# Kernel tuning notes

Measured on AMD Instinct MI355X. Metric: run time of the kernel, lower is better.

Reference implementation:

```python
import jax, jax.numpy as jnp
import numpy as np

N = 100000   # nodes
E = 1600000  # edges (avg degree 16)
IN, H, OUT, P = 100, 256, 256, 128
EPS = 1e-5


def setup_inputs() -> dict:
    key = jax.random.key(0)
    ks = jax.random.split(key, 12)

    def lin(k, o, i):
        return jax.random.normal(k, (o, i), jnp.float32) / np.float32(np.sqrt(i))

    return {
        "x": jax.random.normal(ks[0], (N, IN), jnp.float32),
        "edge_index": jax.random.randint(ks[1], (2, E), 0, N),
        # SAGEConv l (aggregated-neighbor branch, has bias) and r (root branch, no bias)
        "Wl0": lin(ks[2], H, IN), "bl0": jnp.zeros((H,), jnp.float32), "Wr0": lin(ks[3], H, IN),
        "Wl1": lin(ks[4], H, H),  "bl1": jnp.zeros((H,), jnp.float32), "Wr1": lin(ks[5], H, H),
        "Wl2": lin(ks[6], OUT, H), "bl2": jnp.zeros((OUT,), jnp.float32), "Wr2": lin(ks[7], OUT, H),
        # projection head + BatchNorm1d(128)
        "Wp": lin(ks[8], P, OUT), "bp": jnp.zeros((P,), jnp.float32),
        "gamma": jnp.ones((P,), jnp.float32), "beta": jnp.zeros((P,), jnp.float32),
    }


def _sage_conv(x, src, dst, Wl, bl, Wr):
    # PyG SAGEConv default: mean-aggregate source features into destinations,
    # then lin_l(agg) + lin_r(x).
    agg = jax.ops.segment_sum(x[src], dst, num_segments=N)           # [N, d]
    deg = jax.ops.segment_sum(jnp.ones((src.shape[0],), x.dtype), dst, num_segments=N)
    agg = agg / jnp.maximum(deg, 1.0)[:, None]
    return agg @ Wl.T + bl + x @ Wr.T


def reference(x, edge_index, Wl0, bl0, Wr0, Wl1, bl1, Wr1, Wl2, bl2, Wr2, Wp, bp, gamma, beta):
    src, dst = edge_index[0], edge_index[1]
    x = jax.nn.relu(_sage_conv(x, src, dst, Wl0, bl0, Wr0))  # dropout is identity in eval
    x = jax.nn.relu(_sage_conv(x, src, dst, Wl1, bl1, Wr1))
    x = _sage_conv(x, src, dst, Wl2, bl2, Wr2)               # no relu on last layer
    z = x @ Wp.T + bp                                        # projection head -> [N, 128]
    mu = jnp.mean(z, axis=0)
    var = jnp.var(z, axis=0)                                 # biased, as torch BN uses for normalization
    h = gamma * (z - mu) * jax.lax.rsqrt(var + EPS) + beta
    return (x, h)
```

## Files before the change

kernel.cpp:

```cpp
#include <hip/hip_runtime.h>
#include <hip/hip_bf16.h>

#define EPS_BN 1e-5f

using short8  = __attribute__((ext_vector_type(8))) short;
using ushort8 = __attribute__((ext_vector_type(8))) unsigned short;
using f32x4   = __attribute__((ext_vector_type(4))) float;

typedef const __attribute__((address_space(1))) void* gas_ptr;
typedef __attribute__((address_space(3))) void* las_ptr;

__device__ inline float bf2f(unsigned short u) {
    union { unsigned i; float f; } c; c.i = ((unsigned)u) << 16; return c.f;
}
__device__ inline unsigned short f2bf(float f) {
    unsigned x = __float_as_uint(f);
    unsigned r = (x + 0x7FFF + ((x >> 16) & 1)) >> 16;
    return (unsigned short)r;
}

__global__ void zero_i32(int* __restrict__ p, int n) {
    int i = blockIdx.x * blockDim.x + threadIdx.x;
    if (i < n) p[i] = 0;
}
__global__ void zero_f32(float* __restrict__ p, int n) {
    int i = blockIdx.x * blockDim.x + threadIdx.x;
    if (i < n) p[i] = 0.0f;
}

__global__ void zero_rows(unsigned short* __restrict__ xpad,
                          unsigned short* __restrict__ h1,
                          unsigned short* __restrict__ h2, int n) {
    int t = threadIdx.x;
    if (t < 128) xpad[(size_t)n * 128 + t] = 0;
    h1[(size_t)n * 256 + t] = 0;
    h2[(size_t)n * 256 + t] = 0;
}

__global__ void conv_w(const float* __restrict__ w, unsigned short* __restrict__ o,
                       int R, int C, int CP) {
    int t = blockIdx.x * blockDim.x + threadIdx.x;
    if (t >= R * CP) return;
    int r = t / CP, c = t % CP;
    o[t] = (c < C) ? f2bf(w[(size_t)r * C + c]) : (unsigned short)0;
}

__global__ void conv_x_pad(const float* __restrict__ x, unsigned short* __restrict__ xp, int n) {
    int t = blockIdx.x * blockDim.x + threadIdx.x;
    if (t >= n * 32) return;
    int node = t >> 5, g = t & 31;
    int f0 = g * 4;
    ushort4 o;
    const float* xr = x + (size_t)node * 100;
    o.x = (f0 + 0 < 100) ? f2bf(xr[f0 + 0]) : 0;
    o.y = (f0 + 1 < 100) ? f2bf(xr[f0 + 1]) : 0;
    o.z = (f0 + 2 < 100) ? f2bf(xr[f0 + 2]) : 0;
    o.w = (f0 + 3 < 100) ? f2bf(xr[f0 + 3]) : 0;
    *(ushort4*)(xp + (size_t)node * 128 + f0) = o;
}

__global__ void count_k(const int* __restrict__ dst, int* __restrict__ counts, int E) {
    int i = blockIdx.x * blockDim.x + threadIdx.x;
    if (i < E) atomicAdd(&counts[dst[i]], 1);
}

__global__ void scan1(const int* __restrict__ counts, int* __restrict__ rp,
                      int* __restrict__ partials, int n) {
    __shared__ int s[256];
    int t = threadIdx.x;
    int i = blockIdx.x * 256 + t;
    int v = (i < n) ? ((counts[i] + 7) & ~7) : 0;
    s[t] = v;
    __syncthreads();
    for (int off = 1; off < 256; off <<= 1) {
        int u = (t >= off) ? s[t - off] : 0;
        __syncthreads();
        s[t] += u;
        __syncthreads();
    }
    if (i < n) rp[i] = s[t] - v;
    if (t == 255) partials[blockIdx.x] = s[255];
}

__global__ void scan2(int* __restrict__ partials, int nb) {
    __shared__ int s[512];
    int t = threadIdx.x;
    int v = (t < nb) ? partials[t] : 0;
    s[t] = v;
    __syncthreads();
    for (int off = 1; off < 512; off <<= 1) {
        int u = (t >= off) ? s[t - off] : 0;
        __syncthreads();
        s[t] += u;
        __syncthreads();
    }
    if (t < nb) partials[t] = s[t] - v;
}

__global__ void scan3(int* __restrict__ rp, const int* __restrict__ partials, int n) {
    int i = blockIdx.x * blockDim.x + threadIdx.x;
    if (i < n) rp[i] += partials[i >> 8];
}

__global__ void fill_k(const int* __restrict__ src, const int* __restrict__ dst,
                       const int* __restrict__ rp, int* __restrict__ cursor,
                       int* __restrict__ col, int E) {
    int i = blockIdx.x * blockDim.x + threadIdx.x;
    if (i < E) {
        int d = dst[i];
        int pos = atomicAdd(&cursor[d], 1);
        col[rp[d] + pos] = src[i];
    }
}

__global__ void pad_fill(const int* __restrict__ rp, const int* __restrict__ cnt,
                         int* __restrict__ col, int n, int zrow) {
    int node = blockIdx.x * blockDim.x + threadIdx.x;
    if (node >= n) return;
    int d = cnt[node];
    int s = rp[node] + d;
    int e = rp[node] + ((d + 7) & ~7);
    for (int i = s; i < e; ++i) col[i] = zrow;
}

__global__ __launch_bounds__(256) void agg_bf16_256(
    const unsigned short* __restrict__ x, const int* __restrict__ rp,
    const int* __restrict__ cnt, const int* __restrict__ col,
    unsigned short* __restrict__ out, int n) {
    int wave = threadIdx.x >> 6, lane = threadIdx.x & 63;
    int node = blockIdx.x * 4 + wave;
    if (node >= n) return;
    int s = rp[node];
    int deg = cnt[node];
    int nb8 = (deg + 7) >> 3;
    int h = lane >> 5;
    int l32 = lane & 31;
    const size_t coff = (size_t)l32 * 8;

    float a[8] = {0, 0, 0, 0, 0, 0, 0, 0};
    int i = s + h;
    int b = 0;
    for (; b + 2 <= nb8; b += 2, i += 16) {
        int r0 = col[i],     r1 = col[i + 2],  r2 = col[i + 4],  r3 = col[i + 6];
        int r4 = col[i + 8], r5 = col[i + 10], r6 = col[i + 12], r7 = col[i + 14];
        ushort8 v0 = *(const ushort8*)(x + (size_t)r0 * 256 + coff);
        ushort8 v1 = *(const ushort8*)(x + (size_t)r1 * 256 + coff);
        ushort8 v2 = *(const ushort8*)(x + (size_t)r2 * 256 + coff);
        ushort8 v3 = *(const ushort8*)(x + (size_t)r3 * 256 + coff);
        ushort8 v4 = *(const ushort8*)(x + (size_t)r4 * 256 + coff);
        ushort8 v5 = *(const ushort8*)(x + (size_t)r5 * 256 + coff);
        ushort8 v6 = *(const ushort8*)(x + (size_t)r6 * 256 + coff);
        ushort8 v7 = *(const ushort8*)(x + (size_t)r7 * 256 + coff);
#pragma unroll
        for (int j = 0; j < 8; ++j)
            a[j] += ((bf2f(v0[j]) + bf2f(v1[j])) + (bf2f(v2[j]) + bf2f(v3[j]))) +
                    ((bf2f(v4[j]) + bf2f(v5[j])) + (bf2f(v6[j]) + bf2f(v7[j])));
    }
    if (b < nb8) {
        int r0 = col[i], r1 = col[i + 2], r2 = col[i + 4], r3 = col[i + 6];
        ushort8 v0 = *(const ushort8*)(x + (size_t)r0 * 256 + coff);
        ushort8 v1 = *(const ushort8*)(x + (size_t)r1 * 256 + coff);
        ushort8 v2 = *(const ushort8*)(x + (size_t)r2 * 256 + coff);
        ushort8 v3 = *(const ushort8*)(x + (size_t)r3 * 256 + coff);
#pragma unroll
        for (int j = 0; j < 8; ++j)
            a[j] += (bf2f(v0[j]) + bf2f(v1[j])) + (bf2f(v2[j]) + bf2f(v3[j]));
    }
#pragma unroll
    for (int j = 0; j < 8; ++j) a[j] += __shfl_xor(a[j], 32);

    if (h == 0) {
        float sc = 1.0f / fmaxf((float)deg, 1.0f);
        ushort8 o;
#pragma unroll
        for (int j = 0; j < 8; ++j) o[j] = f2bf(a[j] * sc);
        *(ushort8*)(out + (size_t)node * 256 + l32 * 8) = o;
    }
}

__global__ __launch_bounds__(256) void agg_bf16_128(
    const unsigned short* __restrict__ x, const int* __restrict__ rp,
    const int* __restrict__ cnt, const int* __restrict__ col,
    unsigned short* __restrict__ out, int n) {
    int wave = threadIdx.x >> 6, lane = threadIdx.x & 63;
    int node = blockIdx.x * 4 + wave;
    if (node >= n) return;
    int s = rp[node];
    int deg = cnt[node];
    int nb8 = (deg + 7) >> 3;
    int q = lane >> 4;
    int l16 = lane & 15;
    const size_t coff = (size_t)l16 * 8;

    float a[8] = {0, 0, 0, 0, 0, 0, 0, 0};
    int i = s + q;
    int b = 0;
    for (; b + 2 <= nb8; b += 2, i += 16) {
        int r0 = col[i], r1 = col[i + 4], r2 = col[i + 8], r3 = col[i + 12];
        ushort8 v0 = *(const ushort8*)(x + (size_t)r0 * 128 + coff);
        ushort8 v1 = *(const ushort8*)(x + (size_t)r1 * 128 + coff);
        ushort8 v2 = *(const ushort8*)(x + (size_t)r2 * 128 + coff);
        ushort8 v3 = *(const ushort8*)(x + (size_t)r3 * 128 + coff);
#pragma unroll
        for (int j = 0; j < 8; ++j)
            a[j] += (bf2f(v0[j]) + bf2f(v1[j])) + (bf2f(v2[j]) + bf2f(v3[j]));
    }
    if (b < nb8) {
        int r0 = col[i], r1 = col[i + 4];
        ushort8 v0 = *(const ushort8*)(x + (size_t)r0 * 128 + coff);
        ushort8 v1 = *(const ushort8*)(x + (size_t)r1 * 128 + coff);
#pragma unroll
        for (int j = 0; j < 8; ++j) a[j] += bf2f(v0[j]) + bf2f(v1[j]);
    }
#pragma unroll
    for (int j = 0; j < 8; ++j) {
        a[j] += __shfl_xor(a[j], 16);
        a[j] += __shfl_xor(a[j], 32);
    }

    if (lane < 16) {
        float sc = 1.0f / fmaxf((float)deg, 1.0f);
        ushort8 o;
#pragma unroll
        for (int j = 0; j < 8; ++j) o[j] = f2bf(a[j] * sc);
        *(ushort8*)(out + (size_t)node * 128 + l16 * 8) = o;
    }
}

template <int KTOT, int DOUT, bool HAS_AGG, bool RELU, bool STF32, bool STBF16>
__global__ __launch_bounds__(512) void sage_mfma(
    const unsigned short* __restrict__ xp, const unsigned short* __restrict__ ap,
    const unsigned short* __restrict__ Wr, const unsigned short* __restrict__ Wl,
    const float* __restrict__ bias,
    float* __restrict__ outf, unsigned short* __restrict__ outb, int n) {
    constexpr int CT = DOUT / 16;
    constexpr int NSRC = HAS_AGG ? 2 : 1;
    constexpr int FR = DOUT * 4;
    constexpr int CHUNKS = NSRC * CT;
    constexpr int CPW = CHUNKS / 8;
    constexpr int KS = KTOT / 32;
    constexpr int BUFSZ = NSRC * FR * 8;
    __shared__ __align__(16) unsigned short lds[2 * BUFSZ];

    const int t = threadIdx.x;
    const int wave = t >> 6, lane = t & 63;
    const int node0 = blockIdx.x * 128 + wave * 16;
    const bool active = node0 < n;
    const int lcol = lane & 15, lq = lane >> 4;

    auto stage = [&](int ks, int buf) {
        unsigned short* base = lds + buf * BUFSZ;
#pragma unroll
        for (int i = 0; i < CPW; ++i) {
            int chunk = wave * CPW + i;
            int srcSel = chunk / CT, ct = chunk % CT;
            const unsigned short* W = (srcSel == 0) ? Wr : Wl;
            const unsigned short* g = W + (size_t)(ct * 16 + lcol) * KTOT + ks * 32 + lq * 8;
            unsigned short* l = base + chunk * 512;
            __builtin_amdgcn_global_load_lds((gas_ptr)g, (las_ptr)l, 16, 0, 0);
        }
    };

    f32x4 acc[CT];
#pragma unroll
    for (int c = 0; c < CT; ++c) {
        float b = bias[c * 16 + lcol];
        acc[c][0] = b; acc[c][1] = b; acc[c][2] = b; acc[c][3] = b;
    }

    const unsigned short* aRow  = xp + (size_t)(node0 + lcol) * KTOT + lq * 8;
    const unsigned short* aRow2 = HAS_AGG ? (ap + (size_t)(node0 + lcol) * KTOT + lq * 8) : xp;

    stage(0, 0);
    __syncthreads();

    for (int ks = 0; ks < KS; ++ks) {
        if (ks + 1 < KS) stage(ks + 1, (ks + 1) & 1);
        if (active) {
            short8 a = *(const short8*)(aRow + ks * 32);
            const short8* bf = (const short8*)(lds + (ks & 1) * BUFSZ);
#pragma unroll
            for (int c = 0; c < CT; ++c)
                acc[c] = __builtin_amdgcn_mfma_f32_16x16x32_bf16(a, bf[c * 64 + lane], acc[c], 0, 0, 0);
            if (HAS_AGG) {
                short8 a2 = *(const short8*)(aRow2 + ks * 32);
                const short8* bf2 = bf + FR;
#pragma unroll
                for (int c = 0; c < CT; ++c)
                    acc[c] = __builtin_amdgcn_mfma_f32_16x16x32_bf16(a2, bf2[c * 64 + lane], acc[c], 0, 0, 0);
            }
        }
        __syncthreads();
    }
    if (!active) return;

#pragma unroll
    for (int c = 0; c < CT; ++c) {
        f32x4 v = acc[c];
        if (RELU) {
            v[0] = fmaxf(v[0], 0.0f); v[1] = fmaxf(v[1], 0.0f);
            v[2] = fmaxf(v[2], 0.0f); v[3] = fmaxf(v[3], 0.0f);
        }
#pragma unroll
        for (int j = 0; j < 4; ++j) {
            size_t row = (size_t)node0 + lq * 4 + j;
            int colI = c * 16 + lcol;
            if (STF32) outf[row * DOUT + colI] = v[j];
            if (STBF16) outb[row * DOUT + colI] = f2bf(v[j]);
        }
    }
}

__global__ void bn_partial(const float* __restrict__ z, float* __restrict__ sums, int n) {
    int f = threadIdx.x & 127;
    int half = threadIdx.x >> 7;
    float s = 0.0f, s2 = 0.0f;
    for (int row = blockIdx.x * 2 + half; row < n; row += gridDim.x * 2) {
        float v = z[(size_t)row * 128 + f];
        s += v; s2 += v * v;
    }
    __shared__ float ls[256], ls2[256];
    ls[threadIdx.x] = s; ls2[threadIdx.x] = s2;
    __syncthreads();
    if (half == 0) {
        atomicAdd(&sums[f], s + ls[128 + f]);
        atomicAdd(&sums[128 + f], s2 + ls2[128 + f]);
    }
}

__global__ void bn_finalize(const float* __restrict__ sums, const float* __restrict__ gamma,
                            const float* __restrict__ beta, float* __restrict__ params, int n) {
    int f = threadIdx.x;
    float mu = sums[f] / (float)n;
    float var = sums[128 + f] / (float)n - mu * mu;
    float inv = rsqrtf(var + EPS_BN);
    float sc = gamma[f] * inv;
    params[f] = sc;
    params[128 + f] = beta[f] - mu * sc;
}

__global__ void bn_apply(float* __restrict__ z, const float* __restrict__ params, int total4) {
    int i = blockIdx.x * blockDim.x + threadIdx.x;
    for (; i < total4; i += gridDim.x * blockDim.x) {
        float4 v = ((float4*)z)[i];
        int f0 = (i & 31) * 4;
        v.x = v.x * params[f0 + 0] + params[128 + f0 + 0];
        v.y = v.y * params[f0 + 1] + params[128 + f0 + 1];
        v.z = v.z * params[f0 + 2] + params[128 + f0 + 2];
        v.w = v.w * params[f0 + 3] + params[128 + f0 + 3];
        ((float4*)z)[i] = v;
    }
}

extern "C" void kernel_launch(void* const* d_in, const int* in_sizes, int n_in,
                              void* d_out, int out_size, void* d_ws, size_t ws_size,
                              hipStream_t stream) {
    const float* x_in  = (const float*)d_in[0];
    const int*   ei    = (const int*)d_in[1];
    const float* Wl0   = (const float*)d_in[2];
    const float* bl0   = (const float*)d_in[3];
    const float* Wr0   = (const float*)d_in[4];
    const float* Wl1   = (const float*)d_in[5];
    const float* bl1   = (const float*)d_in[6];
    const float* Wr1   = (const float*)d_in[7];
    const float* Wl2   = (const float*)d_in[8];
    const float* bl2   = (const float*)d_in[9];
    const float* Wr2   = (const float*)d_in[10];
    const float* Wp    = (const float*)d_in[11];
    const float* bp    = (const float*)d_in[12];
    const float* gamma = (const float*)d_in[13];
    const float* beta  = (const float*)d_in[14];

    const int IN = 100, INP = 128, H = 256, OUT = 256, P = 128;
    const int n = in_sizes[0] / IN;
    const int E = in_sizes[1] / 2;
    const int* src = ei;
    const int* dst = ei + E;

    size_t off = 0;
    auto alloc = [&](size_t bytes) -> char* {
        char* p = (char*)d_ws + off;
        off += (bytes + 255) & ~(size_t)255;
        return p;
    };
    int*   counts   = (int*)alloc((size_t)n * 4);
    int*   cursor   = (int*)alloc((size_t)n * 4);
    int*   rp       = (int*)alloc((size_t)(n + 1) * 4);
    int*   partials = (int*)alloc(512 * 4);
    int*   col      = (int*)alloc(((size_t)E + 8 * (size_t)n) * 4);
    unsigned short* Wl0b = (unsigned short*)alloc((size_t)H * INP * 2);
    unsigned short* Wr0b = (unsigned short*)alloc((size_t)H * INP * 2);
    unsigned short* Wl1b = (unsigned short*)alloc((size_t)H * H * 2);
    unsigned short* Wr1b = (unsigned short*)alloc((size_t)H * H * 2);
    unsigned short* Wl2b = (unsigned short*)alloc((size_t)OUT * H * 2);
    unsigned short* Wr2b = (unsigned short*)alloc((size_t)OUT * H * 2);
    unsigned short* Wpb  = (unsigned short*)alloc((size_t)P * OUT * 2);
    float* bnsums   = (float*)alloc(256 * 4);
    float* bnparams = (float*)alloc(256 * 4);
    unsigned short* xpad   = (unsigned short*)alloc((size_t)(n + 1) * INP * 2);
    unsigned short* aggpad = (unsigned short*)alloc((size_t)n * INP * 2);
    unsigned short* h1b    = (unsigned short*)alloc((size_t)(n + 1) * H * 2);
    unsigned short* agg1   = (unsigned short*)alloc((size_t)n * H * 2);
    unsigned short* h2b    = (unsigned short*)alloc((size_t)(n + 1) * H * 2);
    (void)alloc((size_t)256 * 512);

    unsigned short* agg2 = h1b;
    unsigned short* xb2  = xpad;

    float* out_x = (float*)d_out;
    float* z     = out_x + (size_t)n * OUT;

    const int nb = (n + 255) / 256;

    zero_i32<<<nb, 256, 0, stream>>>(counts, n);
    zero_i32<<<nb, 256, 0, stream>>>(cursor, n);
    zero_f32<<<1, 256, 0, stream>>>(bnsums, 256);
    count_k<<<(E + 255) / 256, 256, 0, stream>>>(dst, counts, E);
    scan1<<<nb, 256, 0, stream>>>(counts, rp, partials, n);
    scan2<<<1, 512, 0, stream>>>(partials, nb);
    scan3<<<nb, 256, 0, stream>>>(rp, partials, n);
    fill_k<<<(E + 255) / 256, 256, 0, stream>>>(src, dst, rp, cursor, col, E);
    pad_fill<<<nb, 256, 0, stream>>>(rp, counts, col, n, n);

    conv_x_pad<<<(n * 32 + 255) / 256, 256, 0, stream>>>(x_in, xpad, n);
    zero_rows<<<1, 256, 0, stream>>>(xpad, h1b, h2b, n);
    conv_w<<<(H * INP + 255) / 256, 256, 0, stream>>>(Wl0, Wl0b, H, IN, INP);
    conv_w<<<(H * INP + 255) / 256, 256, 0, stream>>>(Wr0, Wr0b, H, IN, INP);
    conv_w<<<(H * H + 255) / 256, 256, 0, stream>>>(Wl1, Wl1b, H, H, H);
    conv_w<<<(H * H + 255) / 256, 256, 0, stream>>>(Wr1, Wr1b, H, H, H);
    conv_w<<<(OUT * H + 255) / 256, 256, 0, stream>>>(Wl2, Wl2b, OUT, H, H);
    conv_w<<<(OUT * H + 255) / 256, 256, 0, stream>>>(Wr2, Wr2b, OUT, H, H);
    conv_w<<<(P * OUT + 255) / 256, 256, 0, stream>>>(Wp, Wpb, P, OUT, OUT);

    const int gemm_grid = (n + 127) / 128;

    agg_bf16_128<<<(n + 3) / 4, 256, 0, stream>>>(xpad, rp, counts, col, aggpad, n);
    sage_mfma<128, 256, true, true, false, true><<<gemm_grid, 512, 0, stream>>>(
        xpad, aggpad, Wr0b, Wl0b, bl0, nullptr, h1b, n);

    agg_bf16_256<<<(n + 3) / 4, 256, 0, stream>>>(h1b, rp, counts, col, agg1, n);
    sage_mfma<256, 256, true, true, false, true><<<gemm_grid, 512, 0, stream>>>(
        h1b, agg1, Wr1b, Wl1b, bl1, nullptr, h2b, n);

    agg_bf16_256<<<(n + 3) / 4, 256, 0, stream>>>(h2b, rp, counts, col, agg2, n);
    sage_mfma<256, 256, true, false, true, true><<<gemm_grid, 512, 0, stream>>>(
        h2b, agg2, Wr2b, Wl2b, bl2, out_x, xb2, n);

    sage_mfma<256, 128, false, false, true, false><<<gemm_grid, 512, 0, stream>>>(
        xb2, nullptr, Wpb, nullptr, bp, z, nullptr, n);

    bn_partial<<<256, 256, 0, stream>>>(z, bnsums, n);
    bn_finalize<<<1, 128, 0, stream>>>(bnsums, gamma, beta, bnparams, n);
    bn_apply<<<2048, 256, 0, stream>>>(z, bnparams, n * (P / 4));
}
```

Measured before the change: 746.6 us.

## Fuse neighbor mean aggregation into SAGE MFMA GEMM kernels

Removes the separate aggregation kernels and computes each node's mean neighbor features directly in registers inside the GEMM kernel, then feeds them into the MFMA as bf16 fragments. This avoids writing and re-reading the aggregated feature buffers through global memory and drops three launches. The cost is a different gather pattern: each lane walks one node's edge list serially, reading 16-byte slices of each neighbor row, so the 16 nodes in a wave run with divergent degrees and less memory-level parallelism. The per-lane register arrays also raise register pressure, and launch bounds are set to 512 threads with a minimum of 4 blocks.

```diff
diff --git a/kernel.cpp b/kernel.cpp
--- a/kernel.cpp
+++ b/kernel.cpp
@@ -123,123 +123,20 @@
     for (int i = s; i < e; ++i) col[i] = zrow;
 }
 
-__global__ __launch_bounds__(256) void agg_bf16_256(
-    const unsigned short* __restrict__ x, const int* __restrict__ rp,
-    const int* __restrict__ cnt, const int* __restrict__ col,
-    unsigned short* __restrict__ out, int n) {
-    int wave = threadIdx.x >> 6, lane = threadIdx.x & 63;
-    int node = blockIdx.x * 4 + wave;
-    if (node >= n) return;
-    int s = rp[node];
-    int deg = cnt[node];
-    int nb8 = (deg + 7) >> 3;
-    int h = lane >> 5;
-    int l32 = lane & 31;
-    const size_t coff = (size_t)l32 * 8;
-
-    float a[8] = {0, 0, 0, 0, 0, 0, 0, 0};
-    int i = s + h;
-    int b = 0;
-    for (; b + 2 <= nb8; b += 2, i += 16) {
-        int r0 = col[i],     r1 = col[i + 2],  r2 = col[i + 4],  r3 = col[i + 6];
-        int r4 = col[i + 8], r5 = col[i + 10], r6 = col[i + 12], r7 = col[i + 14];
-        ushort8 v0 = *(const ushort8*)(x + (size_t)r0 * 256 + coff);
-        ushort8 v1 = *(const ushort8*)(x + (size_t)r1 * 256 + coff);
-        ushort8 v2 = *(const ushort8*)(x + (size_t)r2 * 256 + coff);
-        ushort8 v3 = *(const ushort8*)(x + (size_t)r3 * 256 + coff);
-        ushort8 v4 = *(const ushort8*)(x + (size_t)r4 * 256 + coff);
-        ushort8 v5 = *(const ushort8*)(x + (size_t)r5 * 256 + coff);
-        ushort8 v6 = *(const ushort8*)(x + (size_t)r6 * 256 + coff);
-        ushort8 v7 = *(const ushort8*)(x + (size_t)r7 * 256 + coff);
-#pragma unroll
-        for (int j = 0; j < 8; ++j)
-            a[j] += ((bf2f(v0[j]) + bf2f(v1[j])) + (bf2f(v2[j]) + bf2f(v3[j]))) +
-                    ((bf2f(v4[j]) + bf2f(v5[j])) + (bf2f(v6[j]) + bf2f(v7[j])));
-    }
-    if (b < nb8) {
-        int r0 = col[i], r1 = col[i + 2], r2 = col[i + 4], r3 = col[i + 6];
-        ushort8 v0 = *(const ushort8*)(x + (size_t)r0 * 256 + coff);
-        ushort8 v1 = *(const ushort8*)(x + (size_t)r1 * 256 + coff);
-        ushort8 v2 = *(const ushort8*)(x + (size_t)r2 * 256 + coff);
-        ushort8 v3 = *(const ushort8*)(x + (size_t)r3 * 256 + coff);
-#pragma unroll
-        for (int j = 0; j < 8; ++j)
-            a[j] += (bf2f(v0[j]) + bf2f(v1[j])) + (bf2f(v2[j]) + bf2f(v3[j]));
-    }
-#pragma unroll
-    for (int j = 0; j < 8; ++j) a[j] += __shfl_xor(a[j], 32);
-
-    if (h == 0) {
-        float sc = 1.0f / fmaxf((float)deg, 1.0f);
-        ushort8 o;
-#pragma unroll
-        for (int j = 0; j < 8; ++j) o[j] = f2bf(a[j] * sc);
-        *(ushort8*)(out + (size_t)node * 256 + l32 * 8) = o;
-    }
-}
-
-__global__ __launch_bounds__(256) void agg_bf16_128(
-    const unsigned short* __restrict__ x, const int* __restrict__ rp,
-    const int* __restrict__ cnt, const int* __restrict__ col,
-    unsigned short* __restrict__ out, int n) {
-    int wave = threadIdx.x >> 6, lane = threadIdx.x & 63;
-    int node = blockIdx.x * 4 + wave;
-    if (node >= n) return;
-    int s = rp[node];
-    int deg = cnt[node];
-    int nb8 = (deg + 7) >> 3;
-    int q = lane >> 4;
-    int l16 = lane & 15;
-    const size_t coff = (size_t)l16 * 8;
-
-    float a[8] = {0, 0, 0, 0, 0, 0, 0, 0};
-    int i = s + q;
-    int b = 0;
-    for (; b + 2 <= nb8; b += 2, i += 16) {
-        int r0 = col[i], r1 = col[i + 4], r2 = col[i + 8], r3 = col[i + 12];
-        ushort8 v0 = *(const ushort8*)(x + (size_t)r0 * 128 + coff);
-        ushort8 v1 = *(const ushort8*)(x + (size_t)r1 * 128 + coff);
-        ushort8 v2 = *(const ushort8*)(x + (size_t)r2 * 128 + coff);
-        ushort8 v3 = *(const ushort8*)(x + (size_t)r3 * 128 + coff);
-#pragma unroll
-        for (int j = 0; j < 8; ++j)
-            a[j] += (bf2f(v0[j]) + bf2f(v1[j])) + (bf2f(v2[j]) + bf2f(v3[j]));
-    }
-    if (b < nb8) {
-        int r0 = col[i], r1 = col[i + 4];
-        ushort8 v0 = *(const ushort8*)(x + (size_t)r0 * 128 + coff);
-        ushort8 v1 = *(const ushort8*)(x + (size_t)r1 * 128 + coff);
-#pragma unroll
-        for (int j = 0; j < 8; ++j) a[j] += bf2f(v0[j]) + bf2f(v1[j]);
-    }
-#pragma unroll
-    for (int j = 0; j < 8; ++j) {
-        a[j] += __shfl_xor(a[j], 16);
-        a[j] += __shfl_xor(a[j], 32);
-    }
-
-    if (lane < 16) {
-        float sc = 1.0f / fmaxf((float)deg, 1.0f);
-        ushort8 o;
-#pragma unroll
-        for (int j = 0; j < 8; ++j) o[j] = f2bf(a[j] * sc);
-        *(ushort8*)(out + (size_t)node * 128 + l16 * 8) = o;
-    }
-}
-
 template <int KTOT, int DOUT, bool HAS_AGG, bool RELU, bool STF32, bool STBF16>
-__global__ __launch_bounds__(512) void sage_mfma(
-    const unsigned short* __restrict__ xp, const unsigned short* __restrict__ ap,
+__global__ __launch_bounds__(512, 4) void sage_fused(
+    const unsigned short* __restrict__ xp,
+    const int* __restrict__ rp, const int* __restrict__ cnt, const int* __restrict__ col,
     const unsigned short* __restrict__ Wr, const unsigned short* __restrict__ Wl,
     const float* __restrict__ bias,
     float* __restrict__ outf, unsigned short* __restrict__ outb, int n) {
     constexpr int CT = DOUT / 16;
     constexpr int NSRC = HAS_AGG ? 2 : 1;
-    constexpr int FR = DOUT * 4;
+    constexpr int FR = CT * 64;
     constexpr int CHUNKS = NSRC * CT;
     constexpr int CPW = CHUNKS / 8;
     constexpr int KS = KTOT / 32;
-    constexpr int BUFSZ = NSRC * FR * 8;
+    constexpr int BUFSZ = CHUNKS * 512;
     __shared__ __align__(16) unsigned short lds[2 * BUFSZ];
 
     const int t = threadIdx.x;
@@ -256,10 +153,50 @@
             int srcSel = chunk / CT, ct = chunk % CT;
             const unsigned short* W = (srcSel == 0) ? Wr : Wl;
             const unsigned short* g = W + (size_t)(ct * 16 + lcol) * KTOT + ks * 32 + lq * 8;
-            unsigned short* l = base + chunk * 512;
-            __builtin_amdgcn_global_load_lds((gas_ptr)g, (las_ptr)l, 16, 0, 0);
-        }
+            __builtin_amdgcn_global_load_lds((gas_ptr)g, (las_ptr)(lds + buf * BUFSZ + chunk * 512),
+                                             16, 0, 0);
+        }
+        (void)base;
     };
+
+    stage(0, 0);
+
+    short8 a2f[KS];
+    if constexpr (HAS_AGG) {
+        float aggacc[KS][8];
+#pragma unroll
+        for (int ks = 0; ks < KS; ++ks)
+#pragma unroll
+            for (int j = 0; j < 8; ++j) aggacc[ks][j] = 0.0f;
+        int deg = 0, s = 0;
+        if (active) {
+            int m = node0 + lcol;
+            deg = cnt[m];
+            s = rp[m];
+        }
+        int deg8 = (deg + 7) & ~7;
+        const unsigned short* xq = xp + lq * 8;
+        for (int i = 0; i < deg8; i += 2) {
+            int r0 = col[s + i];
+            int r1 = col[s + i + 1];
+            const unsigned short* row0 = xq + (size_t)r0 * KTOT;
+            const unsigned short* row1 = xq + (size_t)r1 * KTOT;
+#pragma unroll
+            for (int ks = 0; ks < KS; ++ks) {
+                ushort8 v0 = *(const ushort8*)(row0 + ks * 32);
+                ushort8 v1 = *(const ushort8*)(row1 + ks * 32);
+#pragma unroll
+                for (int j = 0; j < 8; ++j)
+                    aggacc[ks][j] += bf2f(v0[j]) + bf2f(v1[j]);
+            }
+        }
+        float sc = 1.0f / fmaxf((float)deg, 1.0f);
+#pragma unroll
+        for (int ks = 0; ks < KS; ++ks)
+#pragma unroll
+            for (int j = 0; j < 8; ++j)
+                a2f[ks][j] = (short)f2bf(aggacc[ks][j] * sc);
+    }
 
     f32x4 acc[CT];
 #pragma unroll
@@ -268,12 +205,11 @@
         acc[c][0] = b; acc[c][1] = b; acc[c][2] = b; acc[c][3] = b;
     }
 
-    const unsigned short* aRow  = xp + (size_t)(node0 + lcol) * KTOT + lq * 8;
-    const unsigned short* aRow2 = HAS_AGG ? (ap + (size_t)(node0 + lcol) * KTOT + lq * 8) : xp;
-
-    stage(0, 0);
+    const unsigned short* aRow = xp + (size_t)(node0 + lcol) * KTOT + lq * 8;
+
     __syncthreads();
 
+#pragma unroll
     for (int ks = 0; ks < KS; ++ks) {
         if (ks + 1 < KS) stage(ks + 1, (ks + 1) & 1);
         if (active) {
@@ -282,12 +218,11 @@
 #pragma unroll
             for (int c = 0; c < CT; ++c)
                 acc[c] = __builtin_amdgcn_mfma_f32_16x16x32_bf16(a, bf[c * 64 + lane], acc[c], 0, 0, 0);
-            if (HAS_AGG) {
-                short8 a2 = *(const short8*)(aRow2 + ks * 32);
+            if constexpr (HAS_AGG) {
                 const short8* bf2 = bf + FR;
 #pragma unroll
                 for (int c = 0; c < CT; ++c)
-                    acc[c] = __builtin_amdgcn_mfma_f32_16x16x32_bf16(a2, bf2[c * 64 + lane], acc[c], 0, 0, 0);
+                    acc[c] = __builtin_amdgcn_mfma_f32_16x16x32_bf16(a2f[ks], bf2[c * 64 + lane], acc[c], 0, 0, 0);
             }
         }
         __syncthreads();
@@ -397,15 +332,11 @@
     unsigned short* Wpb  = (unsigned short*)alloc((size_t)P * OUT * 2);
     float* bnsums   = (float*)alloc(256 * 4);
     float* bnparams = (float*)alloc(256 * 4);
-    unsigned short* xpad   = (unsigned short*)alloc((size_t)(n + 1) * INP * 2);
-    unsigned short* aggpad = (unsigned short*)alloc((size_t)n * INP * 2);
-    unsigned short* h1b    = (unsigned short*)alloc((size_t)(n + 1) * H * 2);
-    unsigned short* agg1   = (unsigned short*)alloc((size_t)n * H * 2);
-    unsigned short* h2b    = (unsigned short*)alloc((size_t)(n + 1) * H * 2);
+    unsigned short* xpad = (unsigned short*)alloc((size_t)(n + 1) * INP * 2);
+    unsigned short* h1b  = (unsigned short*)alloc((size_t)(n + 1) * H * 2);
+    unsigned short* h2b  = (unsigned short*)alloc((size_t)(n + 1) * H * 2);
+    unsigned short* xb2  = (unsigned short*)alloc((size_t)n * H * 2);
     (void)alloc((size_t)256 * 512);
-
-    unsigned short* agg2 = h1b;
-    unsigned short* xb2  = xpad;
 
     float* out_x = (float*)d_out;
     float* z     = out_x + (size_t)n * OUT;
@@ -432,22 +363,19 @@
     conv_w<<<(OUT * H + 255) / 256, 256, 0, stream>>>(Wr2, Wr2b, OUT, H, H);
     conv_w<<<(P * OUT + 255) / 256, 256, 0, stream>>>(Wp, Wpb, P, OUT, OUT);
 
-    const int gemm_grid = (n + 127) / 128;
-
-    agg_bf16_128<<<(n + 3) / 4, 256, 0, stream>>>(xpad, rp, counts, col, aggpad, n);
-    sage_mfma<128, 256, true, true, false, true><<<gemm_grid, 512, 0, stream>>>(
-        xpad, aggpad, Wr0b, Wl0b, bl0, nullptr, h1b, n);
-
-    agg_bf16_256<<<(n + 3) / 4, 256, 0, stream>>>(h1b, rp, counts, col, agg1, n);
-    sage_mfma<256, 256, true, true, false, true><<<gemm_grid, 512, 0, stream>>>(
-        h1b, agg1, Wr1b, Wl1b, bl1, nullptr, h2b, n);
-
-    agg_bf16_256<<<(n + 3) / 4, 256, 0, stream>>>(h2b, rp, counts, col, agg2, n);
-    sage_mfma<256, 256, true, false, true, true><<<gemm_grid, 512, 0, stream>>>(
-        h2b, agg2, Wr2b, Wl2b, bl2, out_x, xb2, n);
-
-    sage_mfma<256, 128, false, false, true, false><<<gemm_grid, 512, 0, stream>>>(
-        xb2, nullptr, Wpb, nullptr, bp, z, nullptr, n);
+    const int gx = (n + 127) / 128;
+
+    sage_fused<128, 256, true, true, false, true><<<gx, 512, 0, stream>>>(
+        xpad, rp, counts, col, Wr0b, Wl0b, bl0, nullptr, h1b, n);
+
+    sage_fused<256, 256, true, true, false, true><<<gx, 512, 0, stream>>>(
+        h1b, rp, counts, col, Wr1b, Wl1b, bl1, nullptr, h2b, n);
+
+    sage_fused<256, 256, true, false, true, true><<<gx, 512, 0, stream>>>(
+        h2b, rp, counts, col, Wr2b, Wl2b, bl2, out_x, xb2, n);
+
+    sage_fused<256, 128, false, false, true, false><<<gx, 512, 0, stream>>>(
+        xb2, rp, counts, col, Wpb, nullptr, bp, z, nullptr, n);
 
     bn_partial<<<256, 256, 0, stream>>>(z, bnsums, n);
     bn_finalize<<<1, 128, 0, stream>>>(bnsums, gamma, beta, bnparams, n);
```

Measured after the change: 1.008 ms. +35.0%, slower.
